# Kernel optimization log

Hardware: AMD Instinct MI355X
Metric: run time of the kernel (lower is better)

## Reference

```python
import jax, jax.numpy as jnp
import numpy as np

N_NODES, N_EDGES, N_GRAPHS = 50000, 800000, 128
D_IN, H1, H2, N_CLASSES = 128, 128, 128, 2
NEG_SLOPE = 0.2  # PyG GATConv default


def setup_inputs() -> dict:
    key = jax.random.key(0)
    ks = jax.random.split(key, 12)
    x = jax.random.normal(ks[0], (N_NODES, D_IN), jnp.float32)
    edge_index = jax.random.randint(ks[1], (2, N_EDGES), 0, N_NODES, jnp.int32)
    batch = jnp.sort(jax.random.randint(ks[2], (N_NODES,), 0, N_GRAPHS, jnp.int32))
    s = 0.05
    return {
        "x": x,
        "W1": jax.random.normal(ks[3], (D_IN, H1), jnp.float32) * s,
        "att_src": jax.random.normal(ks[4], (H1,), jnp.float32) * s,
        "att_dst": jax.random.normal(ks[5], (H1,), jnp.float32) * s,
        "b1": jnp.zeros((H1,), jnp.float32),
        "W2": jax.random.normal(ks[6], (H1, H2), jnp.float32) * s,
        "b2": jnp.zeros((H2,), jnp.float32),
        "Wf": jax.random.normal(ks[7], (H2, N_CLASSES), jnp.float32) * s,
        "bf": jnp.zeros((N_CLASSES,), jnp.float32),
        "edge_index": edge_index,
        "batch": batch,
    }


def _add_self_loops(src, dst, n):
    loop = jnp.arange(n, dtype=src.dtype)
    return jnp.concatenate([src, loop]), jnp.concatenate([dst, loop])


def gat_conv(x, W, att_src, att_dst, bias, src, dst, n):
    h = x @ W  # [N, H1]
    a_src = h @ att_src  # [N]
    a_dst = h @ att_dst  # [N]
    e = a_src[src] + a_dst[dst]  # [E']
    e = jnp.where(e > 0, e, NEG_SLOPE * e)  # leaky_relu
    # softmax over incoming edges of each dst node
    m = jax.ops.segment_max(e, dst, num_segments=n)
    ex = jnp.exp(e - m[dst])
    denom = jax.ops.segment_sum(ex, dst, num_segments=n)
    alpha = ex / denom[dst]  # self loops guarantee denom > 0
    out = jax.ops.segment_sum(alpha[:, None] * h[src], dst, num_segments=n)
    return out + bias


def gcn_conv(x, W, bias, src, dst, n):
    h = x @ W  # [N, H2]
    ones = jnp.ones(src.shape[0], h.dtype)
    deg = jax.ops.segment_sum(ones, dst, num_segments=n)
    dinv = jnp.where(deg > 0, jax.lax.rsqrt(deg), 0.0)
    norm = dinv[src] * dinv[dst]  # [E']
    out = jax.ops.segment_sum(norm[:, None] * h[src], dst, num_segments=n)
    return out + bias


def reference(x, W1, att_src, att_dst, b1, W2, b2, Wf, bf, edge_index, batch):
    n = x.shape[0]
    src, dst = _add_self_loops(edge_index[0], edge_index[1], n)
    h = jax.nn.relu(gat_conv(x, W1, att_src, att_dst, b1, src, dst, n))
    h = jax.nn.relu(gcn_conv(h, W2, b2, src, dst, n))
    # global mean pool over graphs
    sums = jax.ops.segment_sum(h, batch, num_segments=N_GRAPHS)
    cnts = jax.ops.segment_sum(jnp.ones((n,), h.dtype), batch, num_segments=N_GRAPHS)
    rep = sums / jnp.maximum(cnts, 1.0)[:, None]
    return rep @ Wf + bf
```

## Files before the change

kernel.cpp:

```cpp
#include <hip/hip_runtime.h>

#define NN 50000
#define NE 800000
#define EP (NE + NN)
#define NG 128
#define F 128
#define NBE 208
#define EPB 4096
#define NBUCK 196
#define BCAP 6144
#define GB1 782

typedef __attribute__((ext_vector_type(8))) short short8;
typedef __attribute__((ext_vector_type(4))) float float4v;
typedef __attribute__((ext_vector_type(2))) float float2v;
union U8 { uint4 u; short8 s; };

__device__ inline unsigned int bf16rn(float x) {
    unsigned int u = __float_as_uint(x);
    u += 0x7fffu + ((u >> 16) & 1u);
    return u >> 16;
}
__device__ inline unsigned int pack2(float a, float b) {
    return bf16rn(a) | (bf16rn(b) << 16);
}
__device__ inline void bf8_fma2(float2v* acc, float w, uint4 hv) {
    const float2v wv = {w, w};
    float2v p0, p1, p2, p3;
    p0.x = __uint_as_float(hv.x << 16); p0.y = __uint_as_float(hv.x & 0xffff0000u);
    p1.x = __uint_as_float(hv.y << 16); p1.y = __uint_as_float(hv.y & 0xffff0000u);
    p2.x = __uint_as_float(hv.z << 16); p2.y = __uint_as_float(hv.z & 0xffff0000u);
    p3.x = __uint_as_float(hv.w << 16); p3.y = __uint_as_float(hv.w & 0xffff0000u);
    acc[0] += wv * p0;
    acc[1] += wv * p1;
    acc[2] += wv * p2;
    acc[3] += wv * p3;
}

__global__ void pack_wfrag2(const float* __restrict__ W1, const float* __restrict__ W2,
                            uint4* __restrict__ wf, float* __restrict__ gscr,
                            int* __restrict__ cnt) {
    const int p = blockIdx.x * blockDim.x + threadIdx.x;
    if (p >= 4096) {
        const int t = threadIdx.x;
        for (int i = t; i < NG * 32; i += 256) gscr[i] = 0.f;
        for (int i = t; i < NBUCK; i += 256) cnt[i] = 0;
        return;
    }
    const float* W = (p < 2048) ? W1 : W2;
    const int q = p & 2047;
    const int f = q >> 6, l = q & 63;
    const int kt = f >> 3, nt = f & 7;
    const int rb = kt * 32 + ((l >> 4) << 3);
    const int col = nt * 16 + (l & 15);
    const float* wp = W + (size_t)rb * F + col;
    uint4 pk;
    pk.x = pack2(wp[0],     wp[F]);
    pk.y = pack2(wp[2 * F], wp[3 * F]);
    pk.z = pack2(wp[4 * F], wp[5 * F]);
    pk.w = pack2(wp[6 * F], wp[7 * F]);
    wf[p] = pk;
}

__device__ __forceinline__ void gemm1_body(
        const float* __restrict__ Af, const uint4* __restrict__ wf,
        unsigned short* __restrict__ Cb,
        const float* __restrict__ att_src, const float* __restrict__ att_dst,
        float* __restrict__ asrc, float* __restrict__ adst, int bid) {
    const int t = threadIdx.x;
    const int wave = t >> 6, lane = t & 63;
    const int m0 = bid * 64 + wave * 16;
    const int arow = m0 + (lane & 15);
    const int kq = (lane >> 4) << 3;
    U8 a[4];
#pragma unroll
    for (int kt = 0; kt < 4; ++kt) {
        if (arow < NN) {
            const float* ap = Af + (size_t)arow * F + kt * 32 + kq;
            const float4 f0 = *(const float4*)ap;
            const float4 f1 = *(const float4*)(ap + 4);
            a[kt].u = make_uint4(pack2(f0.x, f0.y), pack2(f0.z, f0.w),
                                 pack2(f1.x, f1.y), pack2(f1.z, f1.w));
        } else {
            a[kt].u = make_uint4(0, 0, 0, 0);
        }
    }
    const int ccol = lane & 15;
    const int crow0 = m0 + ((lane >> 4) << 2);
    float ps[4] = {}, pd[4] = {};
    for (int nt = 0; nt < 8; nt += 2) {
        float4v acc0 = {0.f, 0.f, 0.f, 0.f}, acc1 = {0.f, 0.f, 0.f, 0.f};
#pragma unroll
        for (int kt = 0; kt < 4; ++kt) {
            U8 b0, b1;
            b0.u = wf[(kt * 8 + nt) * 64 + lane];
            b1.u = wf[(kt * 8 + nt + 1) * 64 + lane];
            acc0 = __builtin_amdgcn_mfma_f32_16x16x32_bf16(a[kt].s, b0.s, acc0, 0, 0, 0);
            acc1 = __builtin_amdgcn_mfma_f32_16x16x32_bf16(a[kt].s, b1.s, acc1, 0, 0, 0);
        }
#pragma unroll
        for (int r = 0; r < 4; ++r) {
            const int row = crow0 + r;
            if (row < NN) {
                Cb[(size_t)row * F + nt * 16 + ccol]       = (unsigned short)bf16rn(acc0[r]);
                Cb[(size_t)row * F + (nt + 1) * 16 + ccol] = (unsigned short)bf16rn(acc1[r]);
            }
        }
        const float as0 = att_src[nt * 16 + ccol], as1 = att_src[(nt + 1) * 16 + ccol];
        const float ad0 = att_dst[nt * 16 + ccol], ad1 = att_dst[(nt + 1) * 16 + ccol];
#pragma unroll
        for (int r = 0; r < 4; ++r) {
            ps[r] += acc0[r] * as0 + acc1[r] * as1;
            pd[r] += acc0[r] * ad0 + acc1[r] * ad1;
        }
    }
#pragma unroll
    for (int r = 0; r < 4; ++r) {
        float s = ps[r], d = pd[r];
#pragma unroll
        for (int o = 8; o; o >>= 1) { s += __shfl_xor(s, o); d += __shfl_xor(d, o); }
        const int row = crow0 + r;
        if (ccol == 0 && row < NN) { asrc[row] = s; adst[row] = d; }
    }
}

__global__ __launch_bounds__(256) void gemm1_count_scatter(
        const float* __restrict__ x, const uint4* __restrict__ wf1,
        unsigned short* __restrict__ h1b,
        const float* __restrict__ att_src, const float* __restrict__ att_dst,
        float* __restrict__ asrc, float* __restrict__ adst,
        const int* __restrict__ ei, int* __restrict__ cur,
        unsigned int* __restrict__ ebuf) {
    if (blockIdx.x < GB1) {
        gemm1_body(x, wf1, h1b, att_src, att_dst, asrc, adst, blockIdx.x);
        return;
    }
    __shared__ int lcnt[NBUCK];
    __shared__ int lbase[NBUCK];
    const int t = threadIdx.x, b = blockIdx.x - GB1;
    for (int i = t; i < NBUCK; i += 256) lcnt[i] = 0;
    __syncthreads();
    const int e0 = b * EPB;
    int sarr[EPB / 256], darr[EPB / 256];
#pragma unroll
    for (int i = 0; i < EPB / 256; ++i) {
        const int e = e0 + i * 256 + t;
        int s = 0, d = -1;
        if (e < EP) {
            if (e < NE) { s = ei[e]; d = ei[NE + e]; } else { s = d = e - NE; }
            atomicAdd(&lcnt[d >> 8], 1);
        }
        sarr[i] = s; darr[i] = d;
    }
    __syncthreads();
    for (int i = t; i < NBUCK; i += 256) {
        lbase[i] = atomicAdd(&cur[i], lcnt[i]);
        lcnt[i] = 0;
    }
    __syncthreads();
#pragma unroll
    for (int i = 0; i < EPB / 256; ++i) {
        const int d = darr[i];
        if (d >= 0) {
            const int bk = d >> 8;
            const int p = lbase[bk] + atomicAdd(&lcnt[bk], 1);
            ebuf[(size_t)bk * BCAP + p] = (unsigned int)sarr[i] | ((unsigned int)(d & 255) << 16);
        }
    }
}

__global__ void bucket_sort(const unsigned int* __restrict__ ebuf, const int* __restrict__ cnt,
                            int* __restrict__ row_start, unsigned short* __restrict__ csr16,
                            int* __restrict__ deg, float* __restrict__ dinv) {
    __shared__ unsigned int earr[BCAP];
    __shared__ unsigned short out16[BCAP];
    __shared__ int ecnt[256], epre[256];
    const int t = threadIdx.x, g = blockIdx.x;
    const int m = cnt[g];
    const unsigned int* src = ebuf + (size_t)g * BCAP;
    ecnt[t] = 0;
    __syncthreads();
    for (int i = t; i < m; i += 256) {
        const unsigned int v = src[i];
        earr[i] = v;
        atomicAdd(&ecnt[v >> 16], 1);
    }
    __syncthreads();
    const int v0 = ecnt[t];
    epre[t] = v0;
    __syncthreads();
    for (int o = 1; o < 256; o <<= 1) {
        const int u = (t >= o) ? epre[t - o] : 0;
        __syncthreads();
        epre[t] += u;
        __syncthreads();
    }
    const int my_excl = epre[t] - v0;
    const int n = g * 256 + t;
    if (n < NN) {
        row_start[n] = g * BCAP + my_excl;
        deg[n] = v0;
        dinv[n] = rsqrtf((float)v0);
    }
    ecnt[t] = my_excl;
    __syncthreads();
    for (int i = t; i < m; i += 256) {
        const unsigned int v = earr[i];
        const int p = atomicAdd(&ecnt[v >> 16], 1);
        out16[p] = (unsigned short)(v & 0xffffu);
    }
    __syncthreads();
    unsigned short* dst = csr16 + (size_t)g * BCAP;
    for (int i = t; i < m; i += 256) dst[i] = out16[i];
}

__global__ __launch_bounds__(256) void gat_gemm2(
        const int* __restrict__ row_start, const int* __restrict__ deg,
        const unsigned short* __restrict__ csr_src,
        const float* __restrict__ asrc, const float* __restrict__ adst,
        const unsigned short* __restrict__ hb, const float* __restrict__ bias,
        const uint4* __restrict__ wf2, const float* __restrict__ dinv,
        unsigned short* __restrict__ h2b) {
    __shared__ uint4 ldsA[16][17];
    const int lane = threadIdx.x & 63;
    const int qid  = threadIdx.x >> 4;
    const int n    = blockIdx.x * 16 + qid;
    const int lanesub = lane & 15;
    const int qb   = lane & 48;
    const int qo   = lanesub << 3;
    const int lo = row_start[n], hi = lo + deg[n];
    const float adn = adst[n];
    float den = 0.f;
    float2v acc[4];
#pragma unroll
    for (int i = 0; i < 4; ++i) acc[i] = (float2v){0.f, 0.f};
    for (int base = lo; base < hi; base += 16) {
        const int cnt = min(16, hi - base);
        int sv = 0; float ev = 0.f;
        if (lanesub < cnt) {
            sv = csr_src[base + lanesub];
            float sc = asrc[sv] + adn;
            sc = sc > 0.f ? sc : 0.2f * sc;
            ev = __expf(sc);
        }
        den += ev;
        for (int j = 0; j < cnt; j += 8) {
            int ss[8]; float ww[8]; uint4 hh[8];
#pragma unroll
            for (int k = 0; k < 8; ++k) {
                ss[k] = __shfl(sv, qb + j + k);
                ww[k] = __shfl(ev, qb + j + k);
            }
#pragma unroll
            for (int k = 0; k < 8; ++k)
                hh[k] = *(const uint4*)(hb + (size_t)ss[k] * F + qo);
#pragma unroll
            for (int k = 0; k < 8; ++k) bf8_fma2(acc, ww[k], hh[k]);
        }
    }
#pragma unroll
    for (int o = 8; o; o >>= 1) den += __shfl_xor(den, o);
    const float inv = 1.f / den;
    const float4 b0 = *(const float4*)(bias + qo);
    const float4 b1 = *(const float4*)(bias + qo + 4);
    float v[8];
    v[0] = fmaf(acc[0].x, inv, b0.x); v[1] = fmaf(acc[0].y, inv, b0.y);
    v[2] = fmaf(acc[1].x, inv, b0.z); v[3] = fmaf(acc[1].y, inv, b0.w);
    v[4] = fmaf(acc[2].x, inv, b1.x); v[5] = fmaf(acc[2].y, inv, b1.y);
    v[6] = fmaf(acc[3].x, inv, b1.z); v[7] = fmaf(acc[3].y, inv, b1.w);
#pragma unroll
    for (int i = 0; i < 8; ++i) v[i] = v[i] > 0.f ? v[i] : 0.f;
    uint4 pk;
    pk.x = pack2(v[0], v[1]); pk.y = pack2(v[2], v[3]);
    pk.z = pack2(v[4], v[5]); pk.w = pack2(v[6], v[7]);
    ldsA[qid][lanesub] = pk;
    __syncthreads();
    const int wave = threadIdx.x >> 6;
    U8 a[4];
#pragma unroll
    for (int kt = 0; kt < 4; ++kt)
        a[kt].u = ldsA[lane & 15][kt * 4 + (lane >> 4)];
    const int nt = wave * 2;
    float4v acc0 = {0.f, 0.f, 0.f, 0.f}, acc1 = {0.f, 0.f, 0.f, 0.f};
#pragma unroll
    for (int kt = 0; kt < 4; ++kt) {
        U8 b0f, b1f;
        b0f.u = wf2[(kt * 8 + nt) * 64 + lane];
        b1f.u = wf2[(kt * 8 + nt + 1) * 64 + lane];
        acc0 = __builtin_amdgcn_mfma_f32_16x16x32_bf16(a[kt].s, b0f.s, acc0, 0, 0, 0);
        acc1 = __builtin_amdgcn_mfma_f32_16x16x32_bf16(a[kt].s, b1f.s, acc1, 0, 0, 0);
    }
    const int ccol = lane & 15;
    const int crow0 = (lane >> 4) << 2;
#pragma unroll
    for (int r = 0; r < 4; ++r) {
        const int node = blockIdx.x * 16 + crow0 + r;
        const float rs = dinv[node];
        h2b[(size_t)node * F + nt * 16 + ccol]       = (unsigned short)bf16rn(acc0[r] * rs);
        h2b[(size_t)node * F + (nt + 1) * 16 + ccol] = (unsigned short)bf16rn(acc1[r] * rs);
    }
}

__global__ __launch_bounds__(256) void gcn_gather_pool(
        const int* __restrict__ row_start, const int* __restrict__ deg,
        const unsigned short* __restrict__ csr_src,
        const float* __restrict__ dinv, const unsigned short* __restrict__ hb,
        const float* __restrict__ bias, const int* __restrict__ batch,
        const float* __restrict__ Wf, float* __restrict__ gscr) {
    __shared__ int   sg[16];
    __shared__ float sp0[16], sp1[16];
    const int lane = threadIdx.x & 63;
    const int qid  = threadIdx.x >> 4;
    const int n    = blockIdx.x * 16 + qid;
    const int lanesub = lane & 15;
    const int qb   = lane & 48;
    const int qo   = lanesub << 3;
    const int lo = row_start[n], hi = lo + deg[n];
    const float dn = dinv[n];
    float2v acc[4];
#pragma unroll
    for (int i = 0; i < 4; ++i) acc[i] = (float2v){0.f, 0.f};
    for (int base = lo; base < hi; base += 16) {
        const int cnt = min(16, hi - base);
        int sv = 0;
        if (lanesub < cnt) sv = csr_src[base + lanesub];
        for (int j = 0; j < cnt; j += 8) {
            int ss[8]; uint4 hh[8];
#pragma unroll
            for (int k = 0; k < 8; ++k) ss[k] = __shfl(sv, qb + j + k);
#pragma unroll
            for (int k = 0; k < 8; ++k)
                hh[k] = *(const uint4*)(hb + (size_t)ss[k] * F + qo);
#pragma unroll
            for (int k = 0; k < 8; ++k) {
                const float w = (j + k < cnt) ? 1.f : 0.f;
                bf8_fma2(acc, w, hh[k]);
            }
        }
    }
    const float4 b0 = *(const float4*)(bias + qo);
    const float4 b1 = *(const float4*)(bias + qo + 4);
    float v[8];
    v[0] = fmaf(acc[0].x, dn, b0.x); v[1] = fmaf(acc[0].y, dn, b0.y);
    v[2] = fmaf(acc[1].x, dn, b0.z); v[3] = fmaf(acc[1].y, dn, b0.w);
    v[4] = fmaf(acc[2].x, dn, b1.x); v[5] = fmaf(acc[2].y, dn, b1.y);
    v[6] = fmaf(acc[3].x, dn, b1.z); v[7] = fmaf(acc[3].y, dn, b1.w);
#pragma unroll
    for (int i = 0; i < 8; ++i) v[i] = v[i] > 0.f ? v[i] : 0.f;
    const float4 w0 = *(const float4*)(Wf + qo * 2);
    const float4 w1 = *(const float4*)(Wf + qo * 2 + 4);
    const float4 w2 = *(const float4*)(Wf + qo * 2 + 8);
    const float4 w3 = *(const float4*)(Wf + qo * 2 + 12);
    float p0 = v[0]*w0.x + v[1]*w0.z + v[2]*w1.x + v[3]*w1.z +
               v[4]*w2.x + v[5]*w2.z + v[6]*w3.x + v[7]*w3.z;
    float p1 = v[0]*w0.y + v[1]*w0.w + v[2]*w1.y + v[3]*w1.w +
               v[4]*w2.y + v[5]*w2.w + v[6]*w3.y + v[7]*w3.w;
#pragma unroll
    for (int o = 8; o; o >>= 1) { p0 += __shfl_xor(p0, o); p1 += __shfl_xor(p1, o); }
    if (lanesub == 0) { sg[qid] = batch[n]; sp0[qid] = p0; sp1[qid] = p1; }
    __syncthreads();
    if (threadIdx.x == 0) {
#pragma unroll 1
        for (int w = 0; w < 16; ++w) {
            const int g = sg[w];
            if (g < 0) continue;
            float q0 = sp0[w], q1 = sp1[w];
            for (int u = w + 1; u < 16; ++u) {
                if (sg[u] == g) { q0 += sp0[u]; q1 += sp1[u]; sg[u] = -1; }
            }
            atomicAdd(gscr + g * 32,     q0);
            atomicAdd(gscr + g * 32 + 1, q1);
        }
    }
}

__global__ void finalize(const float* __restrict__ gscr, const int* __restrict__ batch,
                         const float* __restrict__ bf, float* __restrict__ out) {
    const int g = threadIdx.x;
    int lo = 0, hi = NN;
    while (lo < hi) { int m = (lo + hi) >> 1; if (batch[m] < g) lo = m + 1; else hi = m; }
    int lo2 = lo, hi2 = NN;
    while (lo2 < hi2) { int m = (lo2 + hi2) >> 1; if (batch[m] < g + 1) lo2 = m + 1; else hi2 = m; }
    const float inv = 1.f / fmaxf((float)(lo2 - lo), 1.f);
    out[g * 2]     = gscr[g * 32]     * inv + bf[0];
    out[g * 2 + 1] = gscr[g * 32 + 1] * inv + bf[1];
}

extern "C" void kernel_launch(void* const* d_in, const int* in_sizes, int n_in,
                              void* d_out, int out_size, void* d_ws, size_t ws_size,
                              hipStream_t stream) {
    const float* x       = (const float*)d_in[0];
    const float* W1      = (const float*)d_in[1];
    const float* att_src = (const float*)d_in[2];
    const float* att_dst = (const float*)d_in[3];
    const float* b1      = (const float*)d_in[4];
    const float* W2      = (const float*)d_in[5];
    const float* b2      = (const float*)d_in[6];
    const float* Wf      = (const float*)d_in[7];
    const float* bf      = (const float*)d_in[8];
    const int*   ei      = (const int*)d_in[9];
    const int*   batch   = (const int*)d_in[10];
    float* out = (float*)d_out;

    unsigned short* h1b  = (unsigned short*)d_ws;
    unsigned short* hgb  = h1b + (size_t)NN * F;
    unsigned short* h2b  = hgb + (size_t)NN * F;
    float* asrc      = (float*)(h2b + (size_t)NN * F);
    float* adst      = asrc + NN;
    float* dinv      = adst + NN;
    float* gscr      = dinv + NN;
    int*   row_start = (int*)(gscr + NG * 32);
    int*   deg       = row_start + NN;
    int*   cnt       = deg + NN;
    unsigned short* csr16 = (unsigned short*)(cnt + NBUCK);
    unsigned int*   ebuf  = (unsigned int*)(csr16 + (size_t)NBUCK * BCAP);
    uint4* wf1       = (uint4*)(ebuf + (size_t)NBUCK * BCAP);
    uint4* wf2       = wf1 + 2048;

    pack_wfrag2<<<17, 256, 0, stream>>>(W1, W2, wf1, gscr, cnt);
    gemm1_count_scatter<<<GB1 + NBE, 256, 0, stream>>>(x, wf1, h1b, att_src, att_dst,
                                                       asrc, adst, ei, cnt, ebuf);
    bucket_sort<<<NBUCK, 256, 0, stream>>>(ebuf, cnt, row_start, csr16, deg, dinv);
    gat_gemm2<<<NN / 16, 256, 0, stream>>>(row_start, deg, csr16, asrc, adst,
                                           h1b, b1, wf2, dinv, h2b);
    gcn_gather_pool<<<NN / 16, 256, 0, stream>>>(row_start, deg, csr16, dinv, h2b, b2,
                                                 batch, Wf, gscr);
    finalize<<<1, NG, 0, stream>>>(gscr, batch, bf, out);
}
```

Measured before the change: 187.5 us.

## Precompute normalized GAT attention weights during bucket sort into packed CSR

Moves the edge score, leaky-relu, exp and softmax normalization from the GAT gather kernel into the bucket sort kernel. That kernel now writes a packed (src, alpha) uint2 array in place of the 16-bit CSR. The goal is to drop the random asrc lookups, the exp work and the denominator shuffle-reduction from the gather loop. In exchange, CSR traffic grows fourfold (8 bytes per edge instead of 2), and the GCN kernel must also read the wider entries. Bucket sort gains a serial per-thread loop over each node's edges, and an extra 24KB LDS array that may lower its occupancy.

```diff
diff --git a/kernel.cpp b/kernel.cpp
--- a/kernel.cpp
+++ b/kernel.cpp
@@ -169,14 +169,20 @@
     }
 }
 
-__global__ void bucket_sort(const unsigned int* __restrict__ ebuf, const int* __restrict__ cnt,
-                            int* __restrict__ row_start, unsigned short* __restrict__ csr16,
-                            int* __restrict__ deg, float* __restrict__ dinv) {
+__global__ __launch_bounds__(256) void bucket_sort(
+        const unsigned int* __restrict__ ebuf, const int* __restrict__ cnt,
+        const float* __restrict__ asrc, const float* __restrict__ adst,
+        int* __restrict__ row_start, uint2* __restrict__ ca,
+        int* __restrict__ deg, float* __restrict__ dinv) {
     __shared__ unsigned int earr[BCAP];
+    __shared__ float evarr[BCAP];
     __shared__ unsigned short out16[BCAP];
     __shared__ int ecnt[256], epre[256];
+    __shared__ float adst_s[256];
     const int t = threadIdx.x, g = blockIdx.x;
     const int m = cnt[g];
+    const int n = g * 256 + t;
+    adst_s[t] = (n < NN) ? adst[n] : 0.f;
     const unsigned int* src = ebuf + (size_t)g * BCAP;
     ecnt[t] = 0;
     __syncthreads();
@@ -196,7 +202,6 @@
         __syncthreads();
     }
     const int my_excl = epre[t] - v0;
-    const int n = g * 256 + t;
     if (n < NN) {
         row_start[n] = g * BCAP + my_excl;
         deg[n] = v0;
@@ -204,20 +209,35 @@
     }
     ecnt[t] = my_excl;
     __syncthreads();
+#pragma unroll 4
     for (int i = t; i < m; i += 256) {
         const unsigned int v = earr[i];
-        const int p = atomicAdd(&ecnt[v >> 16], 1);
-        out16[p] = (unsigned short)(v & 0xffffu);
-    }
-    __syncthreads();
-    unsigned short* dst = csr16 + (size_t)g * BCAP;
-    for (int i = t; i < m; i += 256) dst[i] = out16[i];
+        const int s  = (int)(v & 0xffffu);
+        const int dl = (int)(v >> 16);
+        const int p  = atomicAdd(&ecnt[dl], 1);
+        out16[p] = (unsigned short)s;
+        float sc = asrc[s] + adst_s[dl];
+        sc = sc > 0.f ? sc : 0.2f * sc;
+        evarr[p] = __expf(sc);
+    }
+    __syncthreads();
+    if (n < NN) {
+        uint2* cap = ca + (size_t)g * BCAP;
+        float den = 0.f;
+        for (int k = 0; k < v0; ++k) den += evarr[my_excl + k];
+        const float inv = 1.f / den;
+        for (int k = 0; k < v0; ++k) {
+            uint2 w;
+            w.x = (unsigned int)out16[my_excl + k];
+            w.y = __float_as_uint(evarr[my_excl + k] * inv);
+            cap[my_excl + k] = w;
+        }
+    }
 }
 
 __global__ __launch_bounds__(256) void gat_gemm2(
         const int* __restrict__ row_start, const int* __restrict__ deg,
-        const unsigned short* __restrict__ csr_src,
-        const float* __restrict__ asrc, const float* __restrict__ adst,
+        const uint2* __restrict__ ca,
         const unsigned short* __restrict__ hb, const float* __restrict__ bias,
         const uint4* __restrict__ wf2, const float* __restrict__ dinv,
         unsigned short* __restrict__ h2b) {
@@ -229,8 +249,6 @@
     const int qb   = lane & 48;
     const int qo   = lanesub << 3;
     const int lo = row_start[n], hi = lo + deg[n];
-    const float adn = adst[n];
-    float den = 0.f;
     float2v acc[4];
 #pragma unroll
     for (int i = 0; i < 4; ++i) acc[i] = (float2v){0.f, 0.f};
@@ -238,12 +256,9 @@
         const int cnt = min(16, hi - base);
         int sv = 0; float ev = 0.f;
         if (lanesub < cnt) {
-            sv = csr_src[base + lanesub];
-            float sc = asrc[sv] + adn;
-            sc = sc > 0.f ? sc : 0.2f * sc;
-            ev = __expf(sc);
-        }
-        den += ev;
+            const uint2 e = ca[base + lanesub];
+            sv = (int)e.x; ev = __uint_as_float(e.y);
+        }
         for (int j = 0; j < cnt; j += 8) {
             int ss[8]; float ww[8]; uint4 hh[8];
 #pragma unroll
@@ -258,16 +273,13 @@
             for (int k = 0; k < 8; ++k) bf8_fma2(acc, ww[k], hh[k]);
         }
     }
-#pragma unroll
-    for (int o = 8; o; o >>= 1) den += __shfl_xor(den, o);
-    const float inv = 1.f / den;
     const float4 b0 = *(const float4*)(bias + qo);
     const float4 b1 = *(const float4*)(bias + qo + 4);
     float v[8];
-    v[0] = fmaf(acc[0].x, inv, b0.x); v[1] = fmaf(acc[0].y, inv, b0.y);
-    v[2] = fmaf(acc[1].x, inv, b0.z); v[3] = fmaf(acc[1].y, inv, b0.w);
-    v[4] = fmaf(acc[2].x, inv, b1.x); v[5] = fmaf(acc[2].y, inv, b1.y);
-    v[6] = fmaf(acc[3].x, inv, b1.z); v[7] = fmaf(acc[3].y, inv, b1.w);
+    v[0] = acc[0].x + b0.x; v[1] = acc[0].y + b0.y;
+    v[2] = acc[1].x + b0.z; v[3] = acc[1].y + b0.w;
+    v[4] = acc[2].x + b1.x; v[5] = acc[2].y + b1.y;
+    v[6] = acc[3].x + b1.z; v[7] = acc[3].y + b1.w;
 #pragma unroll
     for (int i = 0; i < 8; ++i) v[i] = v[i] > 0.f ? v[i] : 0.f;
     uint4 pk;
@@ -303,7 +315,7 @@
 
 __global__ __launch_bounds__(256) void gcn_gather_pool(
         const int* __restrict__ row_start, const int* __restrict__ deg,
-        const unsigned short* __restrict__ csr_src,
+        const uint2* __restrict__ ca,
         const float* __restrict__ dinv, const unsigned short* __restrict__ hb,
         const float* __restrict__ bias, const int* __restrict__ batch,
         const float* __restrict__ Wf, float* __restrict__ gscr) {
@@ -323,7 +335,7 @@
     for (int base = lo; base < hi; base += 16) {
         const int cnt = min(16, hi - base);
         int sv = 0;
-        if (lanesub < cnt) sv = csr_src[base + lanesub];
+        if (lanesub < cnt) sv = (int)ca[base + lanesub].x;
         for (int j = 0; j < cnt; j += 8) {
             int ss[8]; uint4 hh[8];
 #pragma unroll
@@ -402,9 +414,12 @@
     const int*   batch   = (const int*)d_in[10];
     float* out = (float*)d_out;
 
-    unsigned short* h1b  = (unsigned short*)d_ws;
-    unsigned short* hgb  = h1b + (size_t)NN * F;
-    unsigned short* h2b  = hgb + (size_t)NN * F;
+    uint4* wf1       = (uint4*)d_ws;
+    uint4* wf2       = wf1 + 2048;
+    uint2* ca        = (uint2*)(wf2 + 2048);
+    unsigned int* ebuf = (unsigned int*)(ca + (size_t)NBUCK * BCAP);
+    unsigned short* h1b = (unsigned short*)(ebuf + (size_t)NBUCK * BCAP);
+    unsigned short* h2b = h1b + (size_t)NN * F;
     float* asrc      = (float*)(h2b + (size_t)NN * F);
     float* adst      = asrc + NN;
     float* dinv      = adst + NN;
@@ -412,18 +427,14 @@
     int*   row_start = (int*)(gscr + NG * 32);
     int*   deg       = row_start + NN;
     int*   cnt       = deg + NN;
-    unsigned short* csr16 = (unsigned short*)(cnt + NBUCK);
-    unsigned int*   ebuf  = (unsigned int*)(csr16 + (size_t)NBUCK * BCAP);
-    uint4* wf1       = (uint4*)(ebuf + (size_t)NBUCK * BCAP);
-    uint4* wf2       = wf1 + 2048;
 
     pack_wfrag2<<<17, 256, 0, stream>>>(W1, W2, wf1, gscr, cnt);
     gemm1_count_scatter<<<GB1 + NBE, 256, 0, stream>>>(x, wf1, h1b, att_src, att_dst,
                                                        asrc, adst, ei, cnt, ebuf);
-    bucket_sort<<<NBUCK, 256, 0, stream>>>(ebuf, cnt, row_start, csr16, deg, dinv);
-    gat_gemm2<<<NN / 16, 256, 0, stream>>>(row_start, deg, csr16, asrc, adst,
-                                           h1b, b1, wf2, dinv, h2b);
-    gcn_gather_pool<<<NN / 16, 256, 0, stream>>>(row_start, deg, csr16, dinv, h2b, b2,
+    bucket_sort<<<NBUCK, 256, 0, stream>>>(ebuf, cnt, asrc, adst,
+                                           row_start, ca, deg, dinv);
+    gat_gemm2<<<NN / 16, 256, 0, stream>>>(row_start, deg, ca, h1b, b1, wf2, dinv, h2b);
+    gcn_gather_pool<<<NN / 16, 256, 0, stream>>>(row_start, deg, ca, dinv, h2b, b2,
                                                  batch, Wf, gscr);
     finalize<<<1, NG, 0, stream>>>(gscr, batch, bf, out);
 }
```

Measured after the change: 194.5 us. 3.8% more time.
